# Kernel optimization log

Hardware: AMD Instinct MI355X
Metric: run time of the kernel (lower is better)

## Reference

```python
import jax, jax.numpy as jnp
import numpy as np

B, N, D, E, K = 4, 4096, 2048, 128, 8


def setup_inputs() -> dict:
    key = jax.random.key(0)
    kx, kw, kb = jax.random.split(key, 3)
    x = jax.random.normal(kx, (B, N, D), dtype=jnp.float32)
    # nn.Linear(input_dim, num_experts): weight [E, D], bias [E]
    bound = 1.0 / np.sqrt(D)
    W = jax.random.uniform(kw, (E, D), dtype=jnp.float32, minval=-bound, maxval=bound)
    b = jax.random.uniform(kb, (E,), dtype=jnp.float32, minval=-bound, maxval=bound)
    return {"x": x, "W": W, "b": b}


def reference(x, W, b):
    # gate logits: [B, N, E]
    gate_logits = jnp.einsum("bnd,ed->bne", x, W) + b
    # top-k over experts
    topk_values, topk_indices = jax.lax.top_k(gate_logits, K)  # [B,N,K]
    topk_gates = jax.nn.softmax(topk_values, axis=-1)          # [B,N,K]
    # scatter normalized gates back into dense [B,N,E]
    onehot = jax.nn.one_hot(topk_indices, E, dtype=topk_gates.dtype)  # [B,N,K,E]
    full_gates = jnp.einsum("bnke,bnk->bne", onehot, topk_gates)
    return full_gates, topk_indices
```

## Files before the change

kernel.cpp:

```cpp
#include <hip/hip_runtime.h>
#include <cfloat>

#define TOKENS 16384
#define DDIM   2048
#define NEXP   128
#define KTOP   8
#define MB     64
#define CH     64
#define NCH    (DDIM / CH)
#define NTHR   512

typedef float    f32x4 __attribute__((ext_vector_type(4)));
typedef _Float16 f16x8 __attribute__((ext_vector_type(8)));

#define WFRAG_N (8 * NCH * 2 * 64)

__device__ __forceinline__ unsigned short f16bits(float f) {
    _Float16 h = (_Float16)f;
    return __builtin_bit_cast(unsigned short, h);
}
__device__ __forceinline__ float f16tof(unsigned short u) {
    return (float)__builtin_bit_cast(_Float16, u);
}

__global__ __launch_bounds__(256, 1) void wfrag_kernel(
    const float* __restrict__ W, uint4* __restrict__ wf)
{
    int id   = blockIdx.x * 256 + threadIdx.x;
    int lane = id & 63;
    int ks   = (id >> 6) & 1;
    int c    = (id >> 7) & (NCH - 1);
    int eb   = id >> 12;
    int e    = eb * 16 + (lane & 15);
    int k0   = c * CH + ks * 32 + (lane >> 4) * 8;
    const float* src = W + (size_t)e * DDIM + k0;
    unsigned hw[4], mw[4];
#pragma unroll
    for (int p = 0; p < 4; ++p) {
        float f0 = src[2 * p], f1 = src[2 * p + 1];
        unsigned short h0 = f16bits(f0), h1 = f16bits(f1);
        unsigned short m0 = f16bits((f0 - f16tof(h0)) * 4096.0f);
        unsigned short m1 = f16bits((f1 - f16tof(h1)) * 4096.0f);
        hw[p] = (unsigned)h0 | ((unsigned)h1 << 16);
        mw[p] = (unsigned)m0 | ((unsigned)m1 << 16);
    }
    wf[id]           = make_uint4(hw[0], hw[1], hw[2], hw[3]);
    wf[WFRAG_N + id] = make_uint4(mw[0], mw[1], mw[2], mw[3]);
}

__device__ __forceinline__ void insert8(float (&vals)[8], int (&idxs)[8], float v, int e) {
    bool c[8];
#pragma unroll
    for (int p = 0; p < 8; ++p) c[p] = v > vals[p];
#pragma unroll
    for (int p = 7; p >= 1; --p) {
        vals[p] = c[p] ? (c[p - 1] ? vals[p - 1] : v) : vals[p];
        idxs[p] = c[p] ? (c[p - 1] ? idxs[p - 1] : e) : idxs[p];
    }
    vals[0] = c[0] ? v : vals[0];
    idxs[0] = c[0] ? e : idxs[0];
}

__global__ __launch_bounds__(NTHR, 1) void router_kernel(
    const float* __restrict__ x, const uint4* __restrict__ wf,
    const float* __restrict__ b, float* __restrict__ out_gates,
    float* __restrict__ out_idx)
{
    __shared__ __align__(16) char smem[66560];
    float* lg  = (float*)smem;
    float* plv = (float*)(smem + 33792);
    int*   pli = (int*)(smem + 50176);

    const int tid  = threadIdx.x;
    const int lane = tid & 63;
    const int wid  = tid >> 6;
    const int tok0 = blockIdx.x * MB;

    const uint4* WFH = wf;
    const uint4* WFM = wf + WFRAG_N;

    f32x4 acc1[4], acc2[4];
#pragma unroll
    for (int mf = 0; mf < 4; ++mf) {
        acc1[mf] = (f32x4){0.f, 0.f, 0.f, 0.f};
        acc2[mf] = (f32x4){0.f, 0.f, 0.f, 0.f};
    }

    const float4* x4 = (const float4*)x;
    const int xr0 = tid >> 4, xr1 = 32 + (tid >> 4), xq = tid & 15;
    const size_t xoff0 = (size_t)(tok0 + xr0) * (DDIM / 4) + xq;
    const size_t xoff1 = (size_t)(tok0 + xr1) * (DDIM / 4) + xq;
    const int xb0 = xr0 * 128 + (((xq >> 1) ^ (xr0 & 7)) << 4) + (xq & 1) * 8;
    const int xb1 = xr1 * 128 + (((xq >> 1) ^ (xr1 & 7)) << 4) + (xq & 1) * 8;

    float4 sxA[2], sxB[2];
    uint4  wA[4], wB[4];

    auto loadW = [&](int c, uint4 (&wreg)[4]) {
#pragma unroll
        for (int ks = 0; ks < 2; ++ks) {
            int idx = ((wid * NCH + c) * 2 + ks) * 64 + lane;
            wreg[ks]     = WFH[idx];
            wreg[2 + ks] = WFM[idx];
        }
    };
    auto convertX = [&](const float4 (&sx)[2], char* ldsDst) {
#pragma unroll
        for (int r = 0; r < 2; ++r) {
            const float4 v = sx[r];
            unsigned short h0 = f16bits(v.x), h1 = f16bits(v.y);
            unsigned short h2 = f16bits(v.z), h3 = f16bits(v.w);
            unsigned short m0 = f16bits((v.x - f16tof(h0)) * 4096.0f);
            unsigned short m1 = f16bits((v.y - f16tof(h1)) * 4096.0f);
            unsigned short m2 = f16bits((v.z - f16tof(h2)) * 4096.0f);
            unsigned short m3 = f16bits((v.w - f16tof(h3)) * 4096.0f);
            uint2 hv = make_uint2((unsigned)h0 | ((unsigned)h1 << 16),
                                  (unsigned)h2 | ((unsigned)h3 << 16));
            uint2 mv = make_uint2((unsigned)m0 | ((unsigned)m1 << 16),
                                  (unsigned)m2 | ((unsigned)m3 << 16));
            const int byteoff = r ? xb1 : xb0;
            *(uint2*)(ldsDst + byteoff)         = hv;
            *(uint2*)(ldsDst + 16384 + byteoff) = mv;
        }
    };

    sxA[0] = x4[xoff0];  sxA[1] = x4[xoff1];
    loadW(0, wA);
    sxB[0] = x4[xoff0 + 16];  sxB[1] = x4[xoff1 + 16];
    convertX(sxA, smem);
    __syncthreads();

    auto step = [&](int c, uint4 (&wCur)[4], uint4 (&wNext)[4],
                    float4 (&sxCur)[2], float4 (&sxNext)[2],
                    char* ldsCur, char* ldsNext) {
        if (c + 2 < NCH) {
            sxNext[0] = x4[xoff0 + (size_t)(c + 2) * 16];
            sxNext[1] = x4[xoff1 + (size_t)(c + 2) * 16];
        }
        if (c + 1 < NCH) loadW(c + 1, wNext);

#pragma unroll
        for (int ks = 0; ks < 2; ++ks) {
            f16x8 ah[4], am[4];
#pragma unroll
            for (int mf = 0; mf < 4; ++mf) {
                int row = 16 * mf + (lane & 15);
                int byteoff = row * 128 +
                    ((((ks << 2) | (lane >> 4)) ^ (row & 7)) << 4);
                ah[mf] = *(const f16x8*)(ldsCur + byteoff);
                am[mf] = *(const f16x8*)(ldsCur + 16384 + byteoff);
            }
            f16x8 wh = __builtin_bit_cast(f16x8, wCur[ks]);
            f16x8 wm = __builtin_bit_cast(f16x8, wCur[2 + ks]);
#pragma unroll
            for (int mf = 0; mf < 4; ++mf) {
                acc1[mf] = __builtin_amdgcn_mfma_f32_16x16x32_f16(
                    ah[mf], wh, acc1[mf], 0, 0, 0);
                acc2[mf] = __builtin_amdgcn_mfma_f32_16x16x32_f16(
                    ah[mf], wm, acc2[mf], 0, 0, 0);
                acc2[mf] = __builtin_amdgcn_mfma_f32_16x16x32_f16(
                    am[mf], wh, acc2[mf], 0, 0, 0);
            }
        }

        if (c + 1 < NCH) convertX(sxCur, ldsNext);
        __syncthreads();
    };

    for (int cc = 0; cc < NCH; cc += 2) {
        step(cc,     wA, wB, sxB, sxA, smem,        smem + 8192);
        step(cc + 1, wB, wA, sxA, sxB, smem + 8192, smem);
    }

    const float bb = b[wid * 16 + (lane & 15)];
#pragma unroll
    for (int mf = 0; mf < 4; ++mf)
#pragma unroll
        for (int r = 0; r < 4; ++r) {
            int t = 16 * mf + (lane >> 4) * 4 + r;
            int e = wid * 16 + (lane & 15);
            lg[t * 132 + e] =
                fmaf(acc2[mf][r], 0.000244140625f, acc1[mf][r]) + bb;
        }
    __syncthreads();

    {
        int tt = tid >> 3, p = tid & 7;
        float vals[8]; int idxs[8];
#pragma unroll
        for (int k = 0; k < 8; ++k) { vals[k] = -FLT_MAX; idxs[k] = 0; }
        const float* row = &lg[tt * 132 + p * 16];
#pragma unroll
        for (int q = 0; q < 16; ++q)
            insert8(vals, idxs, row[q], p * 16 + q);
#pragma unroll
        for (int k = 0; k < 8; ++k) {
            plv[tid * 8 + k] = vals[k];
            pli[tid * 8 + k] = idxs[k];
        }
    }
    __syncthreads();

    float g[8]; int fidx[8];
    const bool active = (tid < MB);
    if (active) {
        float vals[8]; int idxs[8];
#pragma unroll
        for (int k = 0; k < 8; ++k) { vals[k] = -FLT_MAX; idxs[k] = 0; }
        for (int p = 0; p < 8; ++p) {
#pragma unroll
            for (int k = 0; k < 8; ++k)
                insert8(vals, idxs, plv[(tid * 8 + p) * 8 + k], pli[(tid * 8 + p) * 8 + k]);
        }
        float mx = vals[0];
        float s = 0.0f;
#pragma unroll
        for (int k = 0; k < 8; ++k) { g[k] = __expf(vals[k] - mx); s += g[k]; }
        float inv = 1.0f / s;
#pragma unroll
        for (int k = 0; k < 8; ++k) { g[k] *= inv; fidx[k] = idxs[k]; }
#pragma unroll
        for (int k = 0; k < 8; ++k)
            out_idx[(size_t)(tok0 + tid) * KTOP + k] = (float)idxs[k];
    }
    for (int f = tid; f < MB * 132; f += NTHR) lg[f] = 0.0f;
    __syncthreads();

    if (active) {
#pragma unroll
        for (int k = 0; k < 8; ++k) lg[tid * 132 + fidx[k]] = g[k];
    }
    __syncthreads();

    for (int f = tid; f < MB * (NEXP / 4); f += NTHR) {
        int m = f >> 5, e4 = f & 31;
        float4 v = *(const float4*)&lg[m * 132 + e4 * 4];
        ((float4*)out_gates)[(size_t)(tok0 + m) * (NEXP / 4) + e4] = v;
    }
}

extern "C" void kernel_launch(void* const* d_in, const int* in_sizes, int n_in,
                              void* d_out, int out_size, void* d_ws, size_t ws_size,
                              hipStream_t stream) {
    const float* x = (const float*)d_in[0];
    const float* W = (const float*)d_in[1];
    const float* b = (const float*)d_in[2];

    float* out_gates = (float*)d_out;
    float* out_idx   = out_gates + (size_t)TOKENS * NEXP;

    uint4* wf = (uint4*)d_ws;

    wfrag_kernel<<<dim3(WFRAG_N / 256), dim3(256), 0, stream>>>(W, wf);
    router_kernel<<<dim3(TOKENS / MB), dim3(NTHR), 0, stream>>>(x, wf, b, out_gates, out_idx);
}
```

Before: 62.16 us.

## Load X fragments directly into registers and drop LDS staging barriers

```diff
diff --git a/kernel.cpp b/kernel.cpp
--- a/kernel.cpp
+++ b/kernel.cpp
@@ -74,6 +74,8 @@
     const int tid  = threadIdx.x;
     const int lane = tid & 63;
     const int wid  = tid >> 6;
+    const int tg   = wid >> 1;
+    const int eh   = wid & 1;
     const int tok0 = blockIdx.x * MB;
 
     const uint4* WFH = wf;
@@ -81,106 +83,87 @@
 
     f32x4 acc1[4], acc2[4];
 #pragma unroll
-    for (int mf = 0; mf < 4; ++mf) {
-        acc1[mf] = (f32x4){0.f, 0.f, 0.f, 0.f};
-        acc2[mf] = (f32x4){0.f, 0.f, 0.f, 0.f};
+    for (int nf = 0; nf < 4; ++nf) {
+        acc1[nf] = (f32x4){0.f, 0.f, 0.f, 0.f};
+        acc2[nf] = (f32x4){0.f, 0.f, 0.f, 0.f};
     }
 
     const float4* x4 = (const float4*)x;
-    const int xr0 = tid >> 4, xr1 = 32 + (tid >> 4), xq = tid & 15;
-    const size_t xoff0 = (size_t)(tok0 + xr0) * (DDIM / 4) + xq;
-    const size_t xoff1 = (size_t)(tok0 + xr1) * (DDIM / 4) + xq;
-    const int xb0 = xr0 * 128 + (((xq >> 1) ^ (xr0 & 7)) << 4) + (xq & 1) * 8;
-    const int xb1 = xr1 * 128 + (((xq >> 1) ^ (xr1 & 7)) << 4) + (xq & 1) * 8;
-
-    float4 sxA[2], sxB[2];
-    uint4  wA[4], wB[4];
-
-    auto loadW = [&](int c, uint4 (&wreg)[4]) {
+    const size_t xrow4 = (size_t)(tok0 + tg * 16 + (lane & 15)) * (DDIM / 4);
+    const int    xsub  = (lane >> 4) * 2;
+
+    auto loadX = [&](int c, float4 (&xr)[4]) {
+#pragma unroll
+        for (int ks = 0; ks < 2; ++ks)
+#pragma unroll
+            for (int h = 0; h < 2; ++h)
+                xr[ks * 2 + h] = x4[xrow4 + (size_t)c * 16 + ks * 8 + xsub + h];
+    };
+    auto packX = [&](const float4& a, const float4& bq, f16x8& ah, f16x8& am) {
+        float v[8] = {a.x, a.y, a.z, a.w, bq.x, bq.y, bq.z, bq.w};
+        unsigned short hb[8], mb[8];
+#pragma unroll
+        for (int i = 0; i < 8; ++i) {
+            hb[i] = f16bits(v[i]);
+            mb[i] = f16bits((v[i] - f16tof(hb[i])) * 4096.0f);
+        }
+#pragma unroll
+        for (int i = 0; i < 8; ++i) {
+            ah[i] = __builtin_bit_cast(_Float16, hb[i]);
+            am[i] = __builtin_bit_cast(_Float16, mb[i]);
+        }
+    };
+
+    auto computeChunk = [&](int c, const float4 (&xr)[4]) {
+        uint4 wreg[16];
+#pragma unroll
+        for (int ks = 0; ks < 2; ++ks)
+#pragma unroll
+            for (int nf = 0; nf < 4; ++nf) {
+                int idx = (((eh * 4 + nf) * NCH + c) * 2 + ks) * 64 + lane;
+                wreg[ks * 8 + nf * 2]     = WFH[idx];
+                wreg[ks * 8 + nf * 2 + 1] = WFM[idx];
+            }
 #pragma unroll
         for (int ks = 0; ks < 2; ++ks) {
-            int idx = ((wid * NCH + c) * 2 + ks) * 64 + lane;
-            wreg[ks]     = WFH[idx];
-            wreg[2 + ks] = WFM[idx];
+            f16x8 ah, am;
+            packX(xr[ks * 2], xr[ks * 2 + 1], ah, am);
+            __builtin_amdgcn_s_setprio(1);
+#pragma unroll
+            for (int nf = 0; nf < 4; ++nf) {
+                f16x8 wh = __builtin_bit_cast(f16x8, wreg[ks * 8 + nf * 2]);
+                f16x8 wm = __builtin_bit_cast(f16x8, wreg[ks * 8 + nf * 2 + 1]);
+                acc1[nf] = __builtin_amdgcn_mfma_f32_16x16x32_f16(
+                    ah, wh, acc1[nf], 0, 0, 0);
+                acc2[nf] = __builtin_amdgcn_mfma_f32_16x16x32_f16(
+                    ah, wm, acc2[nf], 0, 0, 0);
+                acc2[nf] = __builtin_amdgcn_mfma_f32_16x16x32_f16(
+                    am, wh, acc2[nf], 0, 0, 0);
+            }
+            __builtin_amdgcn_s_setprio(0);
         }
     };
-    auto convertX = [&](const float4 (&sx)[2], char* ldsDst) {
-#pragma unroll
-        for (int r = 0; r < 2; ++r) {
-            const float4 v = sx[r];
-            unsigned short h0 = f16bits(v.x), h1 = f16bits(v.y);
-            unsigned short h2 = f16bits(v.z), h3 = f16bits(v.w);
-            unsigned short m0 = f16bits((v.x - f16tof(h0)) * 4096.0f);
-            unsigned short m1 = f16bits((v.y - f16tof(h1)) * 4096.0f);
-            unsigned short m2 = f16bits((v.z - f16tof(h2)) * 4096.0f);
-            unsigned short m3 = f16bits((v.w - f16tof(h3)) * 4096.0f);
-            uint2 hv = make_uint2((unsigned)h0 | ((unsigned)h1 << 16),
-                                  (unsigned)h2 | ((unsigned)h3 << 16));
-            uint2 mv = make_uint2((unsigned)m0 | ((unsigned)m1 << 16),
-                                  (unsigned)m2 | ((unsigned)m3 << 16));
-            const int byteoff = r ? xb1 : xb0;
-            *(uint2*)(ldsDst + byteoff)         = hv;
-            *(uint2*)(ldsDst + 16384 + byteoff) = mv;
-        }
-    };
-
-    sxA[0] = x4[xoff0];  sxA[1] = x4[xoff1];
-    loadW(0, wA);
-    sxB[0] = x4[xoff0 + 16];  sxB[1] = x4[xoff1 + 16];
-    convertX(sxA, smem);
-    __syncthreads();
-
-    auto step = [&](int c, uint4 (&wCur)[4], uint4 (&wNext)[4],
-                    float4 (&sxCur)[2], float4 (&sxNext)[2],
-                    char* ldsCur, char* ldsNext) {
-        if (c + 2 < NCH) {
-            sxNext[0] = x4[xoff0 + (size_t)(c + 2) * 16];
-            sxNext[1] = x4[xoff1 + (size_t)(c + 2) * 16];
-        }
-        if (c + 1 < NCH) loadW(c + 1, wNext);
-
-#pragma unroll
-        for (int ks = 0; ks < 2; ++ks) {
-            f16x8 ah[4], am[4];
-#pragma unroll
-            for (int mf = 0; mf < 4; ++mf) {
-                int row = 16 * mf + (lane & 15);
-                int byteoff = row * 128 +
-                    ((((ks << 2) | (lane >> 4)) ^ (row & 7)) << 4);
-                ah[mf] = *(const f16x8*)(ldsCur + byteoff);
-                am[mf] = *(const f16x8*)(ldsCur + 16384 + byteoff);
-            }
-            f16x8 wh = __builtin_bit_cast(f16x8, wCur[ks]);
-            f16x8 wm = __builtin_bit_cast(f16x8, wCur[2 + ks]);
-#pragma unroll
-            for (int mf = 0; mf < 4; ++mf) {
-                acc1[mf] = __builtin_amdgcn_mfma_f32_16x16x32_f16(
-                    ah[mf], wh, acc1[mf], 0, 0, 0);
-                acc2[mf] = __builtin_amdgcn_mfma_f32_16x16x32_f16(
-                    ah[mf], wm, acc2[mf], 0, 0, 0);
-                acc2[mf] = __builtin_amdgcn_mfma_f32_16x16x32_f16(
-                    am[mf], wh, acc2[mf], 0, 0, 0);
-            }
-        }
-
-        if (c + 1 < NCH) convertX(sxCur, ldsNext);
-        __syncthreads();
-    };
-
-    for (int cc = 0; cc < NCH; cc += 2) {
-        step(cc,     wA, wB, sxB, sxA, smem,        smem + 8192);
-        step(cc + 1, wB, wA, sxA, sxB, smem + 8192, smem);
-    }
-
-    const float bb = b[wid * 16 + (lane & 15)];
-#pragma unroll
-    for (int mf = 0; mf < 4; ++mf)
+
+    float4 xA[4], xB[4];
+    loadX(0, xA);
+    for (int c = 0; c < NCH; c += 2) {
+        if (c + 1 < NCH) loadX(c + 1, xB);
+        computeChunk(c, xA);
+        if (c + 2 < NCH) loadX(c + 2, xA);
+        computeChunk(c + 1, xB);
+    }
+
+    float bb[4];
+#pragma unroll
+    for (int nf = 0; nf < 4; ++nf) bb[nf] = b[eh * 64 + nf * 16 + (lane & 15)];
+#pragma unroll
+    for (int nf = 0; nf < 4; ++nf)
 #pragma unroll
         for (int r = 0; r < 4; ++r) {
-            int t = 16 * mf + (lane >> 4) * 4 + r;
-            int e = wid * 16 + (lane & 15);
+            int t = tg * 16 + (lane >> 4) * 4 + r;
+            int e = eh * 64 + nf * 16 + (lane & 15);
             lg[t * 132 + e] =
-                fmaf(acc2[mf][r], 0.000244140625f, acc1[mf][r]) + bb;
+                fmaf(acc2[nf][r], 0.000244140625f, acc1[nf][r]) + bb[nf];
         }
     __syncthreads();
 
```

After: 86.97 us. 1.4x slower.
